# Performance work log

Measured on AMD Instinct MI355X. Metric: run time of the kernel, lower is better.

The kernel has to match this reference:

```python
import jax, jax.numpy as jnp
import numpy as np

N = 262144      # samples
D_EMB = 512     # embedding dim
C = 1024        # number of compounds
D_DOSE = 8      # number of dose ranks
MARGIN = 0.1


def setup_inputs() -> dict:
    key = jax.random.key(0)
    k_emb, k_comp, k_dose = jax.random.split(key, 3)
    embeddings = jax.random.normal(k_emb, (N, D_EMB), dtype=jnp.float32)
    compound_labels = jax.random.randint(k_comp, (N,), 0, C, dtype=jnp.int32)
    dose_labels = jax.random.randint(k_dose, (N,), 0, D_DOSE, dtype=jnp.int32)
    return {"embeddings": embeddings, "compound_labels": compound_labels, "dose_labels": dose_labels}


def reference(embeddings, compound_labels, dose_labels):
    # origin = F.normalize(mean(embeddings, dim=0, keepdim=True), dim=-1)
    mu = embeddings.mean(axis=0, keepdims=True)                      # [1, d]
    norm = jnp.maximum(jnp.linalg.norm(mu, axis=-1, keepdims=True), 1e-12)
    origin = mu / norm                                               # [1, d]
    dist = 1.0 - jnp.sum(embeddings * origin, axis=-1)               # [N]

    # fused segment-mean over (compound, dose) grid
    seg = compound_labels.astype(jnp.int32) * D_DOSE + dose_labels.astype(jnp.int32)
    num_seg = C * D_DOSE
    seg_sum = jax.ops.segment_sum(dist, seg, num_segments=num_seg)
    seg_cnt = jax.ops.segment_sum(jnp.ones_like(dist), seg, num_segments=num_seg)
    seg_mean = (seg_sum / jnp.maximum(seg_cnt, 1.0)).reshape(C, D_DOSE)
    present = (seg_cnt > 0).reshape(C, D_DOSE)

    # adjacent present-dose pairs within each compound: sweep dose axis (small, fixed D_DOSE)
    # tracking the last present dose's mean per compound -> same pairs as torch's
    # unique().sort() adjacency over doses actually present.
    last_mean = jnp.zeros((C,), dtype=dist.dtype)
    last_valid = jnp.zeros((C,), dtype=bool)
    loss = jnp.asarray(0.0, dtype=dist.dtype)
    count = jnp.asarray(0.0, dtype=dist.dtype)
    for d in range(D_DOSE):
        cur = seg_mean[:, d]
        pres = present[:, d]
        valid = pres & last_valid
        viol = jnp.maximum(MARGIN - (cur - last_mean), 0.0)          # relu(margin - (d_high - d_low))
        loss = loss + jnp.sum(jnp.where(valid, viol, 0.0))
        count = count + jnp.sum(valid.astype(dist.dtype))
        last_mean = jnp.where(pres, cur, last_mean)
        last_valid = last_valid | pres

    return jnp.where(count > 0, loss / jnp.maximum(count, 1.0), 0.0)
```

## Files before the change

kernel.cpp:

```cpp
#include <hip/hip_runtime.h>
#include <hip/hip_bf16.h>

#define D_EMB    512
#define D4       128
#define NCOMP    1024
#define NDOSE    8
#define NSEG     (NCOMP * NDOSE)
#define MARGIN_F 0.1f

__global__ __launch_bounds__(256) void colsum_kernel(
    const float* __restrict__ emb, float* __restrict__ mu_sum, int n_rows)
{
    const int c4   = threadIdx.x & 127;
    const int rsub = threadIdx.x >> 7;
    const float4* __restrict__ E = (const float4*)emb;

    float4 acc = make_float4(0.f, 0.f, 0.f, 0.f);
    const int stride = gridDim.x * 2;
    #pragma unroll 4
    for (int r = blockIdx.x * 2 + rsub; r < n_rows; r += stride) {
        float4 v = E[(size_t)r * D4 + c4];
        acc.x += v.x; acc.y += v.y; acc.z += v.z; acc.w += v.w;
    }

    __shared__ float4 part[256];
    part[threadIdx.x] = acc;
    __syncthreads();
    if (threadIdx.x < 128) {
        float4 a = part[threadIdx.x];
        float4 b = part[threadIdx.x + 128];
        const int c = c4 * 4;
        atomicAdd(&mu_sum[c + 0], a.x + b.x);
        atomicAdd(&mu_sum[c + 1], a.y + b.y);
        atomicAdd(&mu_sum[c + 2], a.z + b.z);
        atomicAdd(&mu_sum[c + 3], a.w + b.w);
    }
}

__global__ __launch_bounds__(512) void normalize_kernel(
    const float* __restrict__ mu_sum, float* __restrict__ origin, float inv_n)
{
    const int d = threadIdx.x;
    float mu = mu_sum[d] * inv_n;
    float sq = mu * mu;
    #pragma unroll
    for (int off = 32; off; off >>= 1) sq += __shfl_xor(sq, off, 64);
    __shared__ float ws[8];
    const int wave = d >> 6, lane = d & 63;
    if (lane == 0) ws[wave] = sq;
    __syncthreads();
    float ss = 0.f;
    #pragma unroll
    for (int i = 0; i < 8; ++i) ss += ws[i];
    const float norm = fmaxf(sqrtf(ss), 1e-12f);
    origin[d] = mu / norm;
}

__global__ __launch_bounds__(256) void dist_seg_kernel(
    const float* __restrict__ emb, const float* __restrict__ origin,
    const int* __restrict__ comp, const int* __restrict__ dose,
    float* __restrict__ seg_sum, float* __restrict__ seg_cnt, int n_rows)
{
    const int lane = threadIdx.x & 63;
    const int wave = threadIdx.x >> 6;
    const int waves_per_blk = blockDim.x >> 6;
    const int wglob  = blockIdx.x * waves_per_blk + wave;
    const int wtotal = gridDim.x * waves_per_blk;

    const float4* __restrict__ E = (const float4*)emb;
    const float4* __restrict__ O = (const float4*)origin;
    const float4 o0 = O[lane];
    const float4 o1 = O[lane + 64];

    for (int r = wglob; r < n_rows; r += wtotal) {
        const float4* row = E + (size_t)r * D4;
        float4 v0 = row[lane];
        float4 v1 = row[lane + 64];
        float p = v0.x * o0.x + v0.y * o0.y + v0.z * o0.z + v0.w * o0.w
                + v1.x * o1.x + v1.y * o1.y + v1.z * o1.z + v1.w * o1.w;
        #pragma unroll
        for (int off = 32; off; off >>= 1) p += __shfl_xor(p, off, 64);
        if (lane == 0) {
            const float dist = 1.0f - p;
            const int s = comp[r] * NDOSE + dose[r];
            atomicAdd(&seg_sum[s], dist);
            atomicAdd(&seg_cnt[s], 1.0f);
        }
    }
}

__global__ __launch_bounds__(1024) void epilogue_kernel(
    const float* __restrict__ seg_sum, const float* __restrict__ seg_cnt,
    float* __restrict__ out)
{
    const int c = threadIdx.x;
    float loss = 0.f, cnt = 0.f;
    {
        float last_mean = 0.f;
        bool  last_valid = false;
        #pragma unroll
        for (int d = 0; d < NDOSE; ++d) {
            const float s = seg_sum[c * NDOSE + d];
            const float n = seg_cnt[c * NDOSE + d];
            const bool pres = (n > 0.f);
            const float mean = s / fmaxf(n, 1.f);
            if (pres && last_valid) {
                loss += fmaxf(MARGIN_F - (mean - last_mean), 0.f);
                cnt  += 1.f;
            }
            if (pres) { last_mean = mean; last_valid = true; }
        }
    }
    __shared__ float sl[1024];
    __shared__ float sc[1024];
    sl[c] = loss; sc[c] = cnt;
    __syncthreads();
    #pragma unroll
    for (int off = 512; off; off >>= 1) {
        if (c < off) { sl[c] += sl[c + off]; sc[c] += sc[c + off]; }
        __syncthreads();
    }
    if (c == 0) out[0] = (sc[0] > 0.f) ? (sl[0] / fmaxf(sc[0], 1.f)) : 0.f;
}

extern "C" void kernel_launch(void* const* d_in, const int* in_sizes, int n_in,
                              void* d_out, int out_size, void* d_ws, size_t ws_size,
                              hipStream_t stream)
{
    const float* emb  = (const float*)d_in[0];
    const int*   comp = (const int*)d_in[1];
    const int*   dose = (const int*)d_in[2];
    float*       out  = (float*)d_out;

    const int n = in_sizes[1];

    float* seg_sum = (float*)d_ws;
    float* seg_cnt = seg_sum + NSEG;
    float* mu_sum  = seg_cnt + NSEG;
    float* origin  = mu_sum + D_EMB;

    hipMemsetAsync(d_ws, 0, (size_t)(2 * NSEG + D_EMB) * sizeof(float), stream);

    colsum_kernel<<<1024, 256, 0, stream>>>(emb, mu_sum, n);
    normalize_kernel<<<1, 512, 0, stream>>>(mu_sum, origin, 1.0f / (float)n);
    dist_seg_kernel<<<2048, 256, 0, stream>>>(emb, origin, comp, dose,
                                              seg_sum, seg_cnt, n);
    epilogue_kernel<<<1, 1024, 0, stream>>>(seg_sum, seg_cnt, out);
}
```

Before: 851.5 us.

## Replace two embedding passes with counting-sort segment sums and per-segment dot

Rows are bucketed by (compound, dose) with a histogram, scan and scatter. Per-segment embedding sums are then computed once, giving both the global mean and each segment's distance sum via one dot product per segment. This halves the large embedding reads and removes the per-row float atomics. In exchange it adds several small kernels, a permutation buffer, gathered row reads and reassociated float sums.

```diff
diff --git a/kernel.cpp b/kernel.cpp
--- a/kernel.cpp
+++ b/kernel.cpp
@@ -8,33 +8,112 @@
 #define NSEG     (NCOMP * NDOSE)
 #define MARGIN_F 0.1f
 
-__global__ __launch_bounds__(256) void colsum_kernel(
-    const float* __restrict__ emb, float* __restrict__ mu_sum, int n_rows)
-{
+typedef unsigned int uint32;
+
+__global__ __launch_bounds__(256) void hist_kernel(
+    const int* __restrict__ comp, const int* __restrict__ dose,
+    uint32* __restrict__ hist, int n)
+{
+    __shared__ uint32 lh[NSEG];
+    for (int i = threadIdx.x; i < NSEG; i += blockDim.x) lh[i] = 0;
+    __syncthreads();
+    const int stride = gridDim.x * blockDim.x;
+    for (int r = blockIdx.x * blockDim.x + threadIdx.x; r < n; r += stride) {
+        const int s = comp[r] * NDOSE + dose[r];
+        atomicAdd(&lh[s], 1u);
+    }
+    __syncthreads();
+    for (int i = threadIdx.x; i < NSEG; i += blockDim.x) {
+        const uint32 v = lh[i];
+        if (v) atomicAdd(&hist[i], v);
+    }
+}
+
+__global__ __launch_bounds__(1024) void scan_kernel(
+    const uint32* __restrict__ hist, uint32* __restrict__ off,
+    uint32* __restrict__ cur)
+{
+    const int t = threadIdx.x;
+    uint32 v[8];
+    uint32 tot = 0;
+    #pragma unroll
+    for (int j = 0; j < 8; ++j) { v[j] = hist[t * 8 + j]; tot += v[j]; }
+
+    __shared__ uint32 sums[1024];
+    sums[t] = tot;
+    __syncthreads();
+    for (int o = 1; o < 1024; o <<= 1) {
+        uint32 add = (t >= o) ? sums[t - o] : 0u;
+        __syncthreads();
+        sums[t] += add;
+        __syncthreads();
+    }
+    uint32 run = sums[t] - tot;
+    #pragma unroll
+    for (int j = 0; j < 8; ++j) {
+        off[t * 8 + j] = run;
+        cur[t * 8 + j] = run;
+        run += v[j];
+    }
+}
+
+__global__ __launch_bounds__(256) void scatter_kernel(
+    const int* __restrict__ comp, const int* __restrict__ dose,
+    uint32* __restrict__ cur, uint32* __restrict__ perm, int n)
+{
+    const int stride = gridDim.x * blockDim.x;
+    for (int r = blockIdx.x * blockDim.x + threadIdx.x; r < n; r += stride) {
+        const int s = comp[r] * NDOSE + dose[r];
+        const uint32 pos = atomicAdd(&cur[s], 1u);
+        perm[pos] = (uint32)r;
+    }
+}
+
+__global__ __launch_bounds__(256) void segsum_kernel(
+    const float* __restrict__ emb, const uint32* __restrict__ off,
+    const uint32* __restrict__ hist, const uint32* __restrict__ perm,
+    float* __restrict__ S)
+{
+    const int s    = blockIdx.x;
     const int c4   = threadIdx.x & 127;
     const int rsub = threadIdx.x >> 7;
+    const uint32 beg = off[s];
+    const uint32 cnt = hist[s];
     const float4* __restrict__ E = (const float4*)emb;
 
     float4 acc = make_float4(0.f, 0.f, 0.f, 0.f);
-    const int stride = gridDim.x * 2;
-    #pragma unroll 4
-    for (int r = blockIdx.x * 2 + rsub; r < n_rows; r += stride) {
-        float4 v = E[(size_t)r * D4 + c4];
+    for (uint32 i = rsub; i < cnt; i += 2) {
+        const uint32 r = perm[beg + i];
+        const float4 v = E[(size_t)r * D4 + c4];
         acc.x += v.x; acc.y += v.y; acc.z += v.z; acc.w += v.w;
     }
-
     __shared__ float4 part[256];
     part[threadIdx.x] = acc;
     __syncthreads();
     if (threadIdx.x < 128) {
-        float4 a = part[threadIdx.x];
-        float4 b = part[threadIdx.x + 128];
-        const int c = c4 * 4;
-        atomicAdd(&mu_sum[c + 0], a.x + b.x);
-        atomicAdd(&mu_sum[c + 1], a.y + b.y);
-        atomicAdd(&mu_sum[c + 2], a.z + b.z);
-        atomicAdd(&mu_sum[c + 3], a.w + b.w);
-    }
+        const float4 a = part[threadIdx.x];
+        const float4 b = part[threadIdx.x + 128];
+        float4 o;
+        o.x = a.x + b.x; o.y = a.y + b.y; o.z = a.z + b.z; o.w = a.w + b.w;
+        ((float4*)S)[(size_t)s * D4 + c4] = o;
+    }
+}
+
+__global__ __launch_bounds__(128) void musum_kernel(
+    const float* __restrict__ S, float* __restrict__ mu_sum)
+{
+    const int c4 = threadIdx.x;
+    const float4* __restrict__ S4 = (const float4*)S;
+    float4 acc = make_float4(0.f, 0.f, 0.f, 0.f);
+    for (int s = blockIdx.x; s < NSEG; s += gridDim.x) {
+        const float4 v = S4[(size_t)s * D4 + c4];
+        acc.x += v.x; acc.y += v.y; acc.z += v.z; acc.w += v.w;
+    }
+    const int c = c4 * 4;
+    atomicAdd(&mu_sum[c + 0], acc.x);
+    atomicAdd(&mu_sum[c + 1], acc.y);
+    atomicAdd(&mu_sum[c + 2], acc.z);
+    atomicAdd(&mu_sum[c + 3], acc.w);
 }
 
 __global__ __launch_bounds__(512) void normalize_kernel(
@@ -44,7 +123,7 @@
     float mu = mu_sum[d] * inv_n;
     float sq = mu * mu;
     #pragma unroll
-    for (int off = 32; off; off >>= 1) sq += __shfl_xor(sq, off, 64);
+    for (int o = 32; o; o >>= 1) sq += __shfl_xor(sq, o, 64);
     __shared__ float ws[8];
     const int wave = d >> 6, lane = d & 63;
     if (lane == 0) ws[wave] = sq;
@@ -56,68 +135,60 @@
     origin[d] = mu / norm;
 }
 
-__global__ __launch_bounds__(256) void dist_seg_kernel(
-    const float* __restrict__ emb, const float* __restrict__ origin,
-    const int* __restrict__ comp, const int* __restrict__ dose,
-    float* __restrict__ seg_sum, float* __restrict__ seg_cnt, int n_rows)
+__global__ __launch_bounds__(256) void dot_kernel(
+    const float* __restrict__ S, const float* __restrict__ origin,
+    const uint32* __restrict__ hist, float* __restrict__ seg_mean)
 {
     const int lane = threadIdx.x & 63;
     const int wave = threadIdx.x >> 6;
-    const int waves_per_blk = blockDim.x >> 6;
-    const int wglob  = blockIdx.x * waves_per_blk + wave;
-    const int wtotal = gridDim.x * waves_per_blk;
-
-    const float4* __restrict__ E = (const float4*)emb;
-    const float4* __restrict__ O = (const float4*)origin;
+    const int wglob = blockIdx.x * (blockDim.x >> 6) + wave;
+    const int wtot  = gridDim.x * (blockDim.x >> 6);
+    const float4* __restrict__ S4 = (const float4*)S;
+    const float4* __restrict__ O  = (const float4*)origin;
     const float4 o0 = O[lane];
     const float4 o1 = O[lane + 64];
 
-    for (int r = wglob; r < n_rows; r += wtotal) {
-        const float4* row = E + (size_t)r * D4;
-        float4 v0 = row[lane];
-        float4 v1 = row[lane + 64];
+    for (int s = wglob; s < NSEG; s += wtot) {
+        const float4 v0 = S4[(size_t)s * D4 + lane];
+        const float4 v1 = S4[(size_t)s * D4 + lane + 64];
         float p = v0.x * o0.x + v0.y * o0.y + v0.z * o0.z + v0.w * o0.w
                 + v1.x * o1.x + v1.y * o1.y + v1.z * o1.z + v1.w * o1.w;
         #pragma unroll
-        for (int off = 32; off; off >>= 1) p += __shfl_xor(p, off, 64);
+        for (int o = 32; o; o >>= 1) p += __shfl_xor(p, o, 64);
         if (lane == 0) {
-            const float dist = 1.0f - p;
-            const int s = comp[r] * NDOSE + dose[r];
-            atomicAdd(&seg_sum[s], dist);
-            atomicAdd(&seg_cnt[s], 1.0f);
+            const float cntf = (float)hist[s];
+            seg_mean[s] = (cntf - p) / fmaxf(cntf, 1.f);
         }
     }
 }
 
 __global__ __launch_bounds__(1024) void epilogue_kernel(
-    const float* __restrict__ seg_sum, const float* __restrict__ seg_cnt,
+    const float* __restrict__ seg_mean, const uint32* __restrict__ hist,
     float* __restrict__ out)
 {
     const int c = threadIdx.x;
-    float loss = 0.f, cnt = 0.f;
+    float loss = 0.f, cntv = 0.f;
     {
         float last_mean = 0.f;
         bool  last_valid = false;
         #pragma unroll
         for (int d = 0; d < NDOSE; ++d) {
-            const float s = seg_sum[c * NDOSE + d];
-            const float n = seg_cnt[c * NDOSE + d];
-            const bool pres = (n > 0.f);
-            const float mean = s / fmaxf(n, 1.f);
+            const bool  pres = hist[c * NDOSE + d] > 0u;
+            const float mean = seg_mean[c * NDOSE + d];
             if (pres && last_valid) {
                 loss += fmaxf(MARGIN_F - (mean - last_mean), 0.f);
-                cnt  += 1.f;
+                cntv += 1.f;
             }
             if (pres) { last_mean = mean; last_valid = true; }
         }
     }
     __shared__ float sl[1024];
     __shared__ float sc[1024];
-    sl[c] = loss; sc[c] = cnt;
-    __syncthreads();
-    #pragma unroll
-    for (int off = 512; off; off >>= 1) {
-        if (c < off) { sl[c] += sl[c + off]; sc[c] += sc[c + off]; }
+    sl[c] = loss; sc[c] = cntv;
+    __syncthreads();
+    #pragma unroll
+    for (int o = 512; o; o >>= 1) {
+        if (c < o) { sl[c] += sl[c + o]; sc[c] += sc[c + o]; }
         __syncthreads();
     }
     if (c == 0) out[0] = (sc[0] > 0.f) ? (sl[0] / fmaxf(sc[0], 1.f)) : 0.f;
@@ -131,19 +202,25 @@
     const int*   comp = (const int*)d_in[1];
     const int*   dose = (const int*)d_in[2];
     float*       out  = (float*)d_out;
-
     const int n = in_sizes[1];
 
-    float* seg_sum = (float*)d_ws;
-    float* seg_cnt = seg_sum + NSEG;
-    float* mu_sum  = seg_cnt + NSEG;
-    float* origin  = mu_sum + D_EMB;
-
-    hipMemsetAsync(d_ws, 0, (size_t)(2 * NSEG + D_EMB) * sizeof(float), stream);
-
-    colsum_kernel<<<1024, 256, 0, stream>>>(emb, mu_sum, n);
+    uint32* hist    = (uint32*)d_ws;
+    float*  mu_sum  = (float*)(hist + NSEG);
+    uint32* off     = (uint32*)(mu_sum + D_EMB);
+    uint32* cur     = off + NSEG;
+    uint32* perm    = cur + NSEG;
+    float*  seg_mean= (float*)(perm + n);
+    float*  origin  = seg_mean + NSEG;
+    float*  S       = origin + D_EMB;
+
+    hipMemsetAsync(d_ws, 0, (size_t)(NSEG + D_EMB) * sizeof(float), stream);
+
+    hist_kernel    <<<256, 256, 0, stream>>>(comp, dose, hist, n);
+    scan_kernel    <<<1, 1024, 0, stream>>>(hist, off, cur);
+    scatter_kernel <<<1024, 256, 0, stream>>>(comp, dose, cur, perm, n);
+    segsum_kernel  <<<NSEG, 256, 0, stream>>>(emb, off, hist, perm, S);
+    musum_kernel   <<<128, 128, 0, stream>>>(S, mu_sum);
     normalize_kernel<<<1, 512, 0, stream>>>(mu_sum, origin, 1.0f / (float)n);
-    dist_seg_kernel<<<2048, 256, 0, stream>>>(emb, origin, comp, dose,
-                                              seg_sum, seg_cnt, n);
-    epilogue_kernel<<<1, 1024, 0, stream>>>(seg_sum, seg_cnt, out);
-}
+    dot_kernel     <<<128, 256, 0, stream>>>(S, origin, hist, seg_mean);
+    epilogue_kernel<<<1, 1024, 0, stream>>>(seg_mean, hist, out);
+}
```

New measurement: 777.7 us. -8.7%, faster.
